# Performance work log

Hardware: AMD Instinct MI355X
Metric: run time of the kernel (lower is better)

Reference implementation:

```python
import jax, jax.numpy as jnp
import numpy as np

B, SIZE, TRACK = 4096, 1024, 1024  # batch, input size, tracker_size


def setup_inputs() -> dict:
    key = jax.random.key(0)
    ks = jax.random.split(key, 9)
    s = 0.02  # small init scale to keep gates in a sane range
    return {
        "top_buf_h": jax.random.normal(ks[0], (B, SIZE), jnp.float32),
        "top_stack1_h": jax.random.normal(ks[1], (B, SIZE), jnp.float32),
        "top_stack2_h": jax.random.normal(ks[2], (B, SIZE), jnp.float32),
        "h_prev": jax.random.normal(ks[3], (B, TRACK), jnp.float32),
        "c_prev": jax.random.normal(ks[4], (B, TRACK), jnp.float32),
        "W_buf": jax.random.normal(ks[5], (SIZE, 4 * TRACK), jnp.float32) * s,
        "W_stack1": jax.random.normal(ks[6], (SIZE, 4 * TRACK), jnp.float32) * s,
        "W_stack2": jax.random.normal(ks[7], (SIZE, 4 * TRACK), jnp.float32) * s,
        "W_lateral": jax.random.normal(ks[8], (TRACK, 4 * TRACK), jnp.float32) * s,
        "b_lateral": jnp.zeros((4 * TRACK,), jnp.float32),
    }


def reference(top_buf_h, top_stack1_h, top_stack2_h, h_prev, c_prev,
              W_buf, W_stack1, W_stack2, W_lateral, b_lateral):
    # Fused tracker step: 3 bias-free projections + lateral projection (with bias)
    gates = (top_buf_h @ W_buf
             + top_stack1_h @ W_stack1
             + top_stack2_h @ W_stack2
             + h_prev @ W_lateral
             + b_lateral)                      # [B, 4*TRACK]
    # SPINN lstm(c_prev, gates): chunk order (a, i, f, o)
    a, i, f, o = jnp.split(gates, 4, axis=1)
    c = jnp.tanh(a) * jax.nn.sigmoid(i) + jax.nn.sigmoid(f) * c_prev
    h = jax.nn.sigmoid(o) * jnp.tanh(c)
    return (h, c)
```

## Files before the change

### kernel.cpp

```cpp
#include <hip/hip_runtime.h>


typedef __bf16 bf16x8 __attribute__((ext_vector_type(8)));
typedef float  f32x16 __attribute__((ext_vector_type(16)));

__device__ __forceinline__ unsigned short f2bf(float x) {
    unsigned int u = __builtin_bit_cast(unsigned int, x);
    u = (u + 0x7fffu + ((u >> 16) & 1u)) >> 16;
    return (unsigned short)u;
}

__device__ __forceinline__ void gl2lds16(const unsigned short* g, unsigned short* l) {
    __builtin_amdgcn_global_load_lds(
        (const __attribute__((address_space(1))) unsigned int*)g,
        (__attribute__((address_space(3))) unsigned int*)l,
        16, 0, 0);
}

__device__ __forceinline__ float sigf(float x) {
    return __builtin_amdgcn_rcpf(1.f + __expf(-x));
}
__device__ __forceinline__ float tanh_fast(float x) {
    return 2.f * __builtin_amdgcn_rcpf(1.f + __expf(-2.f * x)) - 1.f;
}


__global__ void convert_AB(const float* __restrict__ A0, const float* __restrict__ A1,
                           const float* __restrict__ A2, const float* __restrict__ A3,
                           const float* __restrict__ Wb, const float* __restrict__ W1,
                           const float* __restrict__ W2, const float* __restrict__ Wl,
                           unsigned short* __restrict__ Abf,
                           unsigned short* __restrict__ Bt) {
    __shared__ float t[32][33];
    if (blockIdx.x < 16384) {
        int idx = blockIdx.x * 256 + threadIdx.x;
        int e0  = idx * 4;
        int b   = e0 >> 12;
        int k   = e0 & 4095;
        const float* S = (k < 1024) ? A0 : (k < 2048) ? A1 : (k < 3072) ? A2 : A3;
        int col = k & 1023;
        const float4 v = *reinterpret_cast<const float4*>(S + (size_t)b * 1024 + col);
        ushort4 o;
        o.x = f2bf(v.x); o.y = f2bf(v.y); o.z = f2bf(v.z); o.w = f2bf(v.w);
        *reinterpret_cast<ushort4*>(Abf + (size_t)b * 4096 + k) = o;
    } else {
        int tile = blockIdx.x - 16384;
        int jt = tile & 127, kt = tile >> 7;
        int j0 = jt * 32, k0 = kt * 32;
        int ksel = k0 >> 10;
        const float* S = (ksel == 0) ? Wb : (ksel == 1) ? W1 : (ksel == 2) ? W2 : Wl;
        int kloc = k0 & 1023;
        int tx = threadIdx.x & 31, ty = threadIdx.x >> 5;
#pragma unroll
        for (int i = 0; i < 4; ++i) {
            int r = ty + i * 8;
            t[r][tx] = S[(size_t)(kloc + r) * 4096 + j0 + tx];
        }
        __syncthreads();
        int g = j0 >> 10;
        int nbase = j0 & 1023;
#pragma unroll
        for (int i = 0; i < 4; ++i) {
            int jj = ty + i * 8;
            int u  = nbase + jj;
            int p  = (u >> 5) * 128 + g * 32 + (u & 31);
            Bt[(size_t)p * 4096 + k0 + tx] = f2bf(t[tx][jj]);
        }
    }
}


__global__ __launch_bounds__(512, 2) void gemm_lstm(
        const unsigned short* __restrict__ A,
        const unsigned short* __restrict__ Bt,
        const float* __restrict__ bias,
        const float* __restrict__ cprev,
        float* __restrict__ out) {
    __shared__ unsigned short lds[65536];
#define ASB(b) (lds + (b) * 16384)
#define BSB(b) (lds + 32768 + (b) * 16384)

    const int tid  = threadIdx.x;
    const int wid  = tid >> 6;
    const int lane = tid & 63;
    const int wm = wid >> 1, wn = wid & 1;
    const int l31 = lane & 31, q5 = lane >> 5;
    const int bm = blockIdx.y, bc = blockIdx.x;

    const int X0 = wid * 1024 + lane * 16;
    const int rs = X0 >> 7;
    const int cs = ((X0 & 127) ^ ((rs & 7) << 4)) >> 1;
    const unsigned short* Agb = A  + ((size_t)(bm * 256 + rs)) * 4096 + cs;
    const unsigned short* Bgb = Bt + ((size_t)(bc * 256 + rs)) * 4096 + cs;

    int ca32[4];
#pragma unroll
    for (int ks = 0; ks < 4; ++ks)
        ca32[ks] = ((q5 * 16 + ks * 32) ^ ((lane & 7) << 4)) >> 1;

    f32x16 acc[2][4] = {};

#define STAGE_A(b, h, kt) do {                                               \
        unsigned short* _d = ASB(b) + (h) * 8192 + wid * 512;                \
        const unsigned short* _s = Agb + (size_t)((h) * 128) * 4096 + (kt) * 64; \
        gl2lds16(_s, _d);                                                    \
        gl2lds16(_s + 64 * 4096, _d + 4096);                                 \
    } while (0)
#define STAGE_B(b, h, kt) do {                                               \
        unsigned short* _d = BSB(b) + (h) * 8192 + wid * 512;                \
        const unsigned short* _s = Bgb + (size_t)((h) * 128) * 4096 + (kt) * 64; \
        gl2lds16(_s, _d);                                                    \
        gl2lds16(_s + 64 * 4096, _d + 4096);                                 \
    } while (0)
#define LDA32(buf, mi, cax) (*reinterpret_cast<const bf16x8*>((buf) + (wm * 64 + (mi) * 32 + l31) * 64 + (cax)))
#define LDB32(buf, ni, cax) (*reinterpret_cast<const bf16x8*>((buf) + (wn * 128 + (ni) * 32 + l31) * 64 + (cax)))
#define SBAR() __builtin_amdgcn_s_barrier()
#define VMFENCE() asm volatile("s_waitcnt vmcnt(4)" ::: "memory")

#define KITER(T, PAR) do {                                                   \
        const unsigned short* Ac = ASB(PAR);                                 \
        const unsigned short* Bc = BSB(PAR);                                 \
        const int ktA = ((T) < 63) ? (T) + 1 : 63;                           \
        const int ktB = ((T) < 62) ? (T) + 2 : 63;                           \
        STAGE_A(PAR ^ 1, 0, ktA);                                            \
        STAGE_A(PAR ^ 1, 1, ktA);                                            \
        _Pragma("unroll")                                                    \
        for (int ks = 0; ks < 4; ++ks) {                                     \
            bf16x8 bfr[4];                                                   \
            bf16x8 af[2];                                                    \
            _Pragma("unroll")                                                \
            for (int ni = 0; ni < 4; ++ni) bfr[ni] = LDB32(Bc, ni, ca32[ks]);\
            _Pragma("unroll")                                                \
            for (int m = 0; m < 2; ++m)   af[m] = LDA32(Ac, m, ca32[ks]);    \
            __builtin_amdgcn_s_setprio(1);                                   \
            _Pragma("unroll")                                                \
            for (int m = 0; m < 2; ++m)                                      \
            _Pragma("unroll")                                                \
            for (int ni = 0; ni < 4; ++ni)                                   \
                acc[m][ni] = __builtin_amdgcn_mfma_f32_32x32x16_bf16(        \
                    af[m], bfr[ni], acc[m][ni], 0, 0, 0);                    \
            __builtin_amdgcn_s_setprio(0);                                   \
        }                                                                    \
        asm volatile("s_waitcnt lgkmcnt(0)");                                \
        __builtin_amdgcn_sched_barrier(0);                                   \
        SBAR();    \
        STAGE_B(PAR, 0, ktB);                                                \
        STAGE_B(PAR, 1, ktB);                                                \
        VMFENCE();                                                           \
        SBAR();                          \
    } while (0)

    STAGE_A(0, 0, 0); STAGE_A(0, 1, 0);
    STAGE_B(0, 0, 0); STAGE_B(0, 1, 0);
    STAGE_B(1, 0, 1); STAGE_B(1, 1, 1);
    VMFENCE();
    SBAR();

    for (int u = 0; u < 32; ++u) {
        KITER(2 * u, 0);
        KITER(2 * u + 1, 1);
    }

    const int un = bc * 64 + wn * 32 + l31;
    const float ba  = bias[un];
    const float bi  = bias[1024 + un];
    const float bfv = bias[2048 + un];
    const float bo  = bias[3072 + un];
    float* outh = out;
    float* outc = out + (size_t)4096 * 1024;

#pragma unroll
    for (int mi = 0; mi < 2; ++mi) {
        const int r0 = bm * 256 + wm * 64 + mi * 32 + 4 * q5;
#pragma unroll
        for (int reg = 0; reg < 16; ++reg) {
            const int row = r0 + (reg & 3) + 8 * (reg >> 2);
            const size_t off = (size_t)row * 1024 + un;
            const float a  = acc[mi][0][reg] + ba;
            const float ii = acc[mi][1][reg] + bi;
            const float ff = acc[mi][2][reg] + bfv;
            const float oo = acc[mi][3][reg] + bo;
            const float c  = tanh_fast(a) * sigf(ii) + sigf(ff) * cprev[off];
            outh[off] = sigf(oo) * tanh_fast(c);
            outc[off] = c;
        }
    }
#undef STAGE_A
#undef STAGE_B
#undef LDA32
#undef LDB32
#undef SBAR
#undef VMFENCE
#undef KITER
#undef ASB
#undef BSB
}


extern "C" void kernel_launch(void* const* d_in, const int* in_sizes, int n_in,
                              void* d_out, int out_size, void* d_ws, size_t ws_size,
                              hipStream_t stream) {
    const float* top_buf = (const float*)d_in[0];
    const float* s1      = (const float*)d_in[1];
    const float* s2      = (const float*)d_in[2];
    const float* hprev   = (const float*)d_in[3];
    const float* cprev   = (const float*)d_in[4];
    const float* Wb      = (const float*)d_in[5];
    const float* W1      = (const float*)d_in[6];
    const float* W2      = (const float*)d_in[7];
    const float* Wl      = (const float*)d_in[8];
    const float* bl      = (const float*)d_in[9];

    unsigned short* Abf = (unsigned short*)d_ws;
    unsigned short* Bt  = Abf + (size_t)4096 * 4096;

    convert_AB<<<32768, 256, 0, stream>>>(top_buf, s1, s2, hprev,
                                          Wb, W1, W2, Wl, Abf, Bt);

    dim3 grid(16, 16);
    gemm_lstm<<<grid, 512, 0, stream>>>(Abf, Bt, bl, cprev, (float*)d_out);
}
```

Measured before the change: 164.1 us.

## Switch to 16x16x32 MFMA with 4 waves each computing 128x128 tiles

Cuts the GEMM block from 8 to 4 waves, so each wave now computes a 128x128 sub-tile with an 8x8 grid of 16x16x32 bf16 MFMAs instead of 2x4 32x32 MFMAs. The B weight permutation in the conversion kernel and the LSTM epilogue indexing are rewritten to match the 16-wide gate interleave. Each thread now issues four global-to-LDS loads per stage. This raises register reuse per LDS read but uses 256 accumulator floats per thread, giving one block per CU and a real risk of register pressure or spills and lower latency hiding.

```diff
diff --git a/kernel.cpp b/kernel.cpp
--- a/kernel.cpp
+++ b/kernel.cpp
@@ -2,7 +2,7 @@
 
 
 typedef __bf16 bf16x8 __attribute__((ext_vector_type(8)));
-typedef float  f32x16 __attribute__((ext_vector_type(16)));
+typedef float  f32x4  __attribute__((ext_vector_type(4)));
 
 __device__ __forceinline__ unsigned short f2bf(float x) {
     unsigned int u = __builtin_bit_cast(unsigned int, x);
@@ -63,14 +63,14 @@
         for (int i = 0; i < 4; ++i) {
             int jj = ty + i * 8;
             int u  = nbase + jj;
-            int p  = (u >> 5) * 128 + g * 32 + (u & 31);
+            int p  = (u >> 6) * 256 + ((u >> 5) & 1) * 128 + (g + ((u >> 4) & 1) * 4) * 16 + (u & 15);
             Bt[(size_t)p * 4096 + k0 + tx] = f2bf(t[tx][jj]);
         }
     }
 }
 
 
-__global__ __launch_bounds__(512, 2) void gemm_lstm(
+__global__ __launch_bounds__(256, 1) void gemm_lstm(
         const unsigned short* __restrict__ A,
         const unsigned short* __restrict__ Bt,
         const float* __restrict__ bias,
@@ -84,7 +84,7 @@
     const int wid  = tid >> 6;
     const int lane = tid & 63;
     const int wm = wid >> 1, wn = wid & 1;
-    const int l31 = lane & 31, q5 = lane >> 5;
+    const int lr = lane & 15, lq = lane >> 4;
     const int bm = blockIdx.y, bc = blockIdx.x;
 
     const int X0 = wid * 1024 + lane * 16;
@@ -93,29 +93,32 @@
     const unsigned short* Agb = A  + ((size_t)(bm * 256 + rs)) * 4096 + cs;
     const unsigned short* Bgb = Bt + ((size_t)(bc * 256 + rs)) * 4096 + cs;
 
-    int ca32[4];
-#pragma unroll
-    for (int ks = 0; ks < 4; ++ks)
-        ca32[ks] = ((q5 * 16 + ks * 32) ^ ((lane & 7) << 4)) >> 1;
-
-    f32x16 acc[2][4] = {};
+    const int swz = (lr & 7) << 4;
+    const int ca0 = ((lq * 16) ^ swz) >> 1;
+    const int ca1 = ((64 + lq * 16) ^ swz) >> 1;
+
+    f32x4 acc[8][8] = {};
 
 #define STAGE_A(b, h, kt) do {                                               \
         unsigned short* _d = ASB(b) + (h) * 8192 + wid * 512;                \
         const unsigned short* _s = Agb + (size_t)((h) * 128) * 4096 + (kt) * 64; \
-        gl2lds16(_s, _d);                                                    \
-        gl2lds16(_s + 64 * 4096, _d + 4096);                                 \
+        gl2lds16(_s,                 _d);                                    \
+        gl2lds16(_s + 32 * 4096,     _d + 2048);                             \
+        gl2lds16(_s + 64 * 4096,     _d + 4096);                             \
+        gl2lds16(_s + 96 * 4096,     _d + 6144);                             \
     } while (0)
 #define STAGE_B(b, h, kt) do {                                               \
         unsigned short* _d = BSB(b) + (h) * 8192 + wid * 512;                \
         const unsigned short* _s = Bgb + (size_t)((h) * 128) * 4096 + (kt) * 64; \
-        gl2lds16(_s, _d);                                                    \
-        gl2lds16(_s + 64 * 4096, _d + 4096);                                 \
+        gl2lds16(_s,                 _d);                                    \
+        gl2lds16(_s + 32 * 4096,     _d + 2048);                             \
+        gl2lds16(_s + 64 * 4096,     _d + 4096);                             \
+        gl2lds16(_s + 96 * 4096,     _d + 6144);                             \
     } while (0)
-#define LDA32(buf, mi, cax) (*reinterpret_cast<const bf16x8*>((buf) + (wm * 64 + (mi) * 32 + l31) * 64 + (cax)))
-#define LDB32(buf, ni, cax) (*reinterpret_cast<const bf16x8*>((buf) + (wn * 128 + (ni) * 32 + l31) * 64 + (cax)))
+#define LDA(buf, mi, cax) (*reinterpret_cast<const bf16x8*>((buf) + (wm * 128 + (mi) * 16 + lr) * 64 + (cax)))
+#define LDB(buf, ni, cax) (*reinterpret_cast<const bf16x8*>((buf) + (wn * 128 + (ni) * 16 + lr) * 64 + (cax)))
 #define SBAR() __builtin_amdgcn_s_barrier()
-#define VMFENCE() asm volatile("s_waitcnt vmcnt(4)" ::: "memory")
+#define VMFENCE() asm volatile("s_waitcnt vmcnt(8)" ::: "memory")
 
 #define KITER(T, PAR) do {                                                   \
         const unsigned short* Ac = ASB(PAR);                                 \
@@ -125,25 +128,24 @@
         STAGE_A(PAR ^ 1, 0, ktA);                                            \
         STAGE_A(PAR ^ 1, 1, ktA);                                            \
         _Pragma("unroll")                                                    \
-        for (int ks = 0; ks < 4; ++ks) {                                     \
-            bf16x8 bfr[4];                                                   \
-            bf16x8 af[2];                                                    \
-            _Pragma("unroll")                                                \
-            for (int ni = 0; ni < 4; ++ni) bfr[ni] = LDB32(Bc, ni, ca32[ks]);\
-            _Pragma("unroll")                                                \
-            for (int m = 0; m < 2; ++m)   af[m] = LDA32(Ac, m, ca32[ks]);    \
+        for (int ks = 0; ks < 2; ++ks) {                                     \
+            const int cax = ks ? ca1 : ca0;                                  \
+            bf16x8 af[8], bfr[8];                                            \
+            _Pragma("unroll")                                                \
+            for (int m = 0; m < 8; ++m)  af[m]  = LDA(Ac, m, cax);           \
+            _Pragma("unroll")                                                \
+            for (int n = 0; n < 8; ++n)  bfr[n] = LDB(Bc, n, cax);           \
             __builtin_amdgcn_s_setprio(1);                                   \
             _Pragma("unroll")                                                \
-            for (int m = 0; m < 2; ++m)                                      \
-            _Pragma("unroll")                                                \
-            for (int ni = 0; ni < 4; ++ni)                                   \
-                acc[m][ni] = __builtin_amdgcn_mfma_f32_32x32x16_bf16(        \
-                    af[m], bfr[ni], acc[m][ni], 0, 0, 0);                    \
+            for (int m = 0; m < 8; ++m)                                      \
+            _Pragma("unroll")                                                \
+            for (int n = 0; n < 8; ++n)                                      \
+                acc[m][n] = __builtin_amdgcn_mfma_f32_16x16x32_bf16(         \
+                    af[m], bfr[n], acc[m][n], 0, 0, 0);                      \
             __builtin_amdgcn_s_setprio(0);                                   \
         }                                                                    \
         asm volatile("s_waitcnt lgkmcnt(0)");                                \
-        __builtin_amdgcn_sched_barrier(0);                                   \
-        SBAR();    \
+        SBAR();        \
         STAGE_B(PAR, 0, ktB);                                                \
         STAGE_B(PAR, 1, ktB);                                                \
         VMFENCE();                                                           \
@@ -161,34 +163,37 @@
         KITER(2 * u + 1, 1);
     }
 
-    const int un = bc * 64 + wn * 32 + l31;
-    const float ba  = bias[un];
-    const float bi  = bias[1024 + un];
-    const float bfv = bias[2048 + un];
-    const float bo  = bias[3072 + un];
+    const int u0 = bc * 64 + wn * 32 + lr;
     float* outh = out;
     float* outc = out + (size_t)4096 * 1024;
 
 #pragma unroll
-    for (int mi = 0; mi < 2; ++mi) {
-        const int r0 = bm * 256 + wm * 64 + mi * 32 + 4 * q5;
-#pragma unroll
-        for (int reg = 0; reg < 16; ++reg) {
-            const int row = r0 + (reg & 3) + 8 * (reg >> 2);
-            const size_t off = (size_t)row * 1024 + un;
-            const float a  = acc[mi][0][reg] + ba;
-            const float ii = acc[mi][1][reg] + bi;
-            const float ff = acc[mi][2][reg] + bfv;
-            const float oo = acc[mi][3][reg] + bo;
-            const float c  = tanh_fast(a) * sigf(ii) + sigf(ff) * cprev[off];
-            outh[off] = sigf(oo) * tanh_fast(c);
-            outc[off] = c;
+    for (int hi = 0; hi < 2; ++hi) {
+        const int un = u0 + hi * 16;
+        const float ba  = bias[un];
+        const float bi  = bias[1024 + un];
+        const float bfv = bias[2048 + un];
+        const float bo  = bias[3072 + un];
+#pragma unroll
+        for (int mi = 0; mi < 8; ++mi) {
+            const int r0 = bm * 256 + wm * 128 + mi * 16 + lq * 4;
+#pragma unroll
+            for (int r = 0; r < 4; ++r) {
+                const size_t off = (size_t)(r0 + r) * 1024 + un;
+                const float a  = acc[mi][hi * 4 + 0][r] + ba;
+                const float ii = acc[mi][hi * 4 + 1][r] + bi;
+                const float ff = acc[mi][hi * 4 + 2][r] + bfv;
+                const float oo = acc[mi][hi * 4 + 3][r] + bo;
+                const float c  = tanh_fast(a) * sigf(ii) + sigf(ff) * cprev[off];
+                outh[off] = sigf(oo) * tanh_fast(c);
+                outc[off] = c;
+            }
         }
     }
 #undef STAGE_A
 #undef STAGE_B
-#undef LDA32
-#undef LDB32
+#undef LDA
+#undef LDB
 #undef SBAR
 #undef VMFENCE
 #undef KITER
@@ -218,5 +223,5 @@
                                           Wb, W1, W2, Wl, Abf, Bt);
 
     dim3 grid(16, 16);
-    gemm_lstm<<<grid, 512, 0, stream>>>(Abf, Bt, bl, cprev, (float*)d_out);
-}
+    gemm_lstm<<<grid, 256, 0, stream>>>(Abf, Bt, bl, cprev, (float*)d_out);
+}
```

Result: slower. 218.7 us (+33.3%).
